# Kernel tuning notes

Hardware: AMD Instinct MI355X
Metric: run time of the kernel (lower is better)

Reference implementation:

```python
import jax, jax.numpy as jnp
import numpy as np

B, DIM, H, W = 4, 192, 256, 256
HEADS, DS = 6, 2
CPH = DIM // HEADS  # channels per head = 32
DN = ('NCHW', 'OIHW', 'NCHW')


def _conv(x, w, padding, groups=1):
    return jax.lax.conv_general_dilated(x, w, (1, 1), padding,
                                        dimension_numbers=DN,
                                        feature_group_count=groups)


def setup_inputs() -> dict:
    key = jax.random.key(0)
    ks = jax.random.split(key, 5)
    x = jax.random.normal(ks[0], (B, DIM, H, W), dtype=jnp.float32)
    temperature = jnp.ones((HEADS, 1, 1), dtype=jnp.float32)
    qkv_w = jax.random.normal(ks[1], (3 * DIM, DIM, 1, 1), dtype=jnp.float32) * 0.02
    dw_w = jax.random.normal(ks[2], (3 * DIM, 1, 3, 3), dtype=jnp.float32) * 0.02
    proj_w = jax.random.normal(ks[3], (DIM, DIM, 1, 1), dtype=jnp.float32) * 0.02
    a = jnp.full((1,), 0.2, dtype=jnp.float32)
    return {"x": x, "temperature": temperature, "qkv_w": qkv_w, "dw_w": dw_w,
            "proj_w": proj_w, "a1": a, "a2": a, "a3": a, "a4": a}


def _masked_softmax(attn, kk):
    # top-k mask per row (exact torch.topk + scatter_ semantics)
    _, idx = jax.lax.top_k(attn, kk)                      # [b,h,C,kk]
    mask = jax.nn.one_hot(idx, attn.shape[-1], dtype=jnp.bool_).any(axis=-2)
    return jax.nn.softmax(jnp.where(mask, attn, -jnp.inf), axis=-1)


def reference(x, temperature, qkv_w, dw_w, proj_w, a1, a2, a3, a4):
    b, c, h, w = x.shape
    h2, w2 = h // DS, w // DS
    # 1x1 qkv conv at full res, then exact adaptive (regular) max pool by DS
    qkv = _conv(x, qkv_w, 'VALID')                        # [b, 3*dim, h, w]
    qkv = jax.lax.reduce_window(qkv, -jnp.inf, jax.lax.max,
                                (1, 1, DS, DS), (1, 1, DS, DS), 'VALID')
    # depthwise 3x3
    qkv = _conv(qkv, dw_w, 'SAME', groups=3 * DIM)        # [b, 3*dim, h2, w2]
    q, k, v = jnp.split(qkv, 3, axis=1)
    n = h2 * w2
    q = q.reshape(b, HEADS, CPH, n)
    k = k.reshape(b, HEADS, CPH, n)
    v = v.reshape(b, HEADS, CPH, n)
    # F.normalize along last dim (eps clamp 1e-12)
    q = q / jnp.maximum(jnp.linalg.norm(q, axis=-1, keepdims=True), 1e-12)
    k = k / jnp.maximum(jnp.linalg.norm(k, axis=-1, keepdims=True), 1e-12)
    attn = jnp.einsum('bhcn,bhdn->bhcd', q, k) * temperature[None]  # [b,h,C,C]
    Cc = attn.shape[-1]
    att1 = _masked_softmax(attn, Cc // 2)
    att2 = _masked_softmax(attn, Cc * 2 // 3)
    att3 = _masked_softmax(attn, Cc * 3 // 4)
    att4 = _masked_softmax(attn, Cc * 4 // 5)
    def apply(a):
        return jnp.einsum('bhcd,bhdn->bhcn', a, v)
    out = apply(att1) * a1 + apply(att2) * a2 + apply(att3) * a3 + apply(att4) * a4
    out = out.reshape(b, DIM, h2, w2)
    out = jax.nn.gelu(out, approximate=False)
    # nearest upsample by integer factor DS
    out = jnp.repeat(jnp.repeat(out, DS, axis=2), DS, axis=3)
    out = _conv(out, proj_w, 'VALID')
    return out
```

## Files before the change

### kernel.cpp

```cpp
#include <hip/hip_runtime.h>
#include <hip/hip_bf16.h>
#include <math.h>

typedef __attribute__((ext_vector_type(8))) short bf16x8;
typedef __attribute__((ext_vector_type(4))) float f32x4;
typedef __attribute__((ext_vector_type(4))) unsigned int u32x4;

#define NP 16384
#define HWFULL 65536

__device__ __forceinline__ unsigned short f2bf(float f){
    union { float f; unsigned int u; } v; v.f = f;
    unsigned int u = v.u;
    u += 0x7fffu + ((u >> 16) & 1u);
    return (unsigned short)(u >> 16);
}
__device__ __forceinline__ float bf2f(unsigned short h){
    union { unsigned int u; float f; } v; v.u = ((unsigned int)h) << 16;
    return v.f;
}
__device__ __forceinline__ unsigned int pk2(float a, float b){
    unsigned int r;
    asm("v_cvt_pk_bf16_f32 %0, %1, %2" : "=v"(r) : "v"(a), "v"(b));
    return r;
}

__global__ void k_convert(const float* __restrict__ s, unsigned short* __restrict__ d, int n){
    int i = blockIdx.x * 256 + threadIdx.x;
    if (i < n) d[i] = f2bf(s[i]);
}

__global__ __launch_bounds__(256, 2)
void k_qkvpool(const float* __restrict__ x, const unsigned short* __restrict__ Wbf,
               unsigned short* __restrict__ qkvp){
    __shared__ unsigned short Bl[128*200];
    __shared__ unsigned short Ep[192*36];
    int tid = threadIdx.x;
    int lane = tid & 63, wv = tid >> 6;
    int n16 = lane & 15, quad = lane >> 4;
    int bx = blockIdx.x;
    int y2 = bx >> 2, x2blk = bx & 3;
    int b = blockIdx.y;

    #pragma unroll 6
    for (int j=0;j<12;j++){
        int idx = tid + j*256;
        int g = idx >> 7, w = idx & 127;
        int y = y2*2 + (w >> 6);
        int xc = x2blk*64 + (w & 63);
        const float* xp = x + (size_t)(b*192 + g*8) * HWFULL + y*256 + xc;
        float v0 = xp[0];
        float v1 = xp[(size_t)1*HWFULL];
        float v2 = xp[(size_t)2*HWFULL];
        float v3 = xp[(size_t)3*HWFULL];
        float v4 = xp[(size_t)4*HWFULL];
        float v5 = xp[(size_t)5*HWFULL];
        float v6 = xp[(size_t)6*HWFULL];
        float v7 = xp[(size_t)7*HWFULL];
        u32x4 pk;
        pk.x = pk2(v0,v1); pk.y = pk2(v2,v3); pk.z = pk2(v4,v5); pk.w = pk2(v6,v7);
        *(u32x4*)&Bl[w*200 + g*8] = pk;
    }
    bf16x8 afc[3], afn[3];
    #pragma unroll
    for (int j=0;j<3;j++)
        afc[j] = *(const bf16x8*)(Wbf + (size_t)(((wv*3+j)*16 + n16)*192 + quad*8));
    __syncthreads();

    for (int ocblk=0; ocblk<3; ocblk++){
        f32x4 acc[3][8];
        #pragma unroll
        for (int j=0;j<3;j++)
          #pragma unroll
          for (int s=0;s<8;s++)
            acc[j][s] = (f32x4){0.f,0.f,0.f,0.f};

        #pragma unroll 1
        for (int it=0; it<6; it++){
            int nocb = (it==5) ? ocblk+1 : ocblk;
            int nit  = (it==5) ? 0 : it+1;
            if (nocb < 3){
                #pragma unroll
                for (int j=0;j<3;j++)
                    afn[j] = *(const bf16x8*)(Wbf +
                        (size_t)((nocb*192 + (wv*3+j)*16 + n16)*192 + nit*32 + quad*8));
            }
            int bko = it*32 + quad*8;
            bf16x8 bfr[8];
            #pragma unroll
            for (int s=0;s<8;s++) bfr[s] = *(const bf16x8*)&Bl[(s*16 + n16)*200 + bko];
            #pragma unroll
            for (int j=0;j<3;j++)
              #pragma unroll
              for (int s=0;s<8;s++)
                acc[j][s] = __builtin_amdgcn_mfma_f32_16x16x32_bf16(afc[j], bfr[s], acc[j][s], 0,0,0);
            #pragma unroll
            for (int j=0;j<3;j++) afc[j] = afn[j];
        }
        __syncthreads();
        #pragma unroll
        for (int j=0;j<3;j++){
            int ocr = (wv*3+j)*16 + quad*4;
            #pragma unroll
            for (int sp=0;sp<4;sp++){
                #pragma unroll
                for (int r=0;r<4;r++){
                    float v = fmaxf(acc[j][sp][r], acc[j][sp+4][r]);
                    float o = __shfl_xor(v, 1, 64);
                    v = fmaxf(v, o);
                    if ((n16 & 1) == 0)
                        Ep[(ocr + r)*36 + sp*8 + (n16 >> 1)] = f2bf(v);
                }
            }
        }
        __syncthreads();
        size_t rowbase = (size_t)(b*576 + ocblk*192)*NP + y2*128 + x2blk*32;
        #pragma unroll
        for (int it2=0; it2<6; it2++){
            int c = tid + it2*256;
            int row = c >> 3, seg = c & 7;
            uint2 vv = *(const uint2*)&Ep[row*36 + seg*4];
            *(uint2*)(qkvp + rowbase + (size_t)row*NP + seg*4) = vv;
        }
    }
}

__global__ void k_dwconv(const unsigned short* __restrict__ qkvp, const float* __restrict__ dww,
                         unsigned short* __restrict__ dwoutB, float* __restrict__ sumsq){
    __shared__ float sl[18*132];
    int tid = threadIdx.x;
    int y0 = blockIdx.x * 16;
    int ch = blockIdx.y;
    int b  = blockIdx.z;
    const unsigned short* in = qkvp + (size_t)(b*576 + ch) * NP;
    int l = tid & 63, wr = tid >> 6;
    #pragma unroll
    for (int j=0;j<5;j++){
        int row = wr + j*4;
        if (row < 18){
            int gy = y0 - 1 + row;
            float2 v = make_float2(0.f, 0.f);
            if (gy >= 0 && gy < 128){
                unsigned int u = *(const unsigned int*)&in[gy*128 + l*2];
                v.x = bf2f((unsigned short)(u & 0xffffu));
                v.y = bf2f((unsigned short)(u >> 16));
            }
            *(float2*)&sl[row*132 + 2 + l*2] = v;
        }
    }
    if (tid < 18) sl[tid*132 + 1] = 0.f;
    else if (tid < 36) sl[(tid-18)*132 + 130] = 0.f;
    float w0 = dww[ch*9+0], w1 = dww[ch*9+1], w2 = dww[ch*9+2];
    float w3 = dww[ch*9+3], w4 = dww[ch*9+4], w5 = dww[ch*9+5];
    float w6 = dww[ch*9+6], w7 = dww[ch*9+7], w8 = dww[ch*9+8];
    __syncthreads();
    unsigned short* outp = dwoutB + (size_t)(b*576 + ch) * NP;
    int col = tid & 127, half = tid >> 7;
    float ssq = 0.f;
    int base = (half*8)*132 + col + 1;
    float r0a=sl[base],     r0b=sl[base+1],   r0c=sl[base+2];
    float r1a=sl[base+132], r1b=sl[base+133], r1c=sl[base+134];
    #pragma unroll
    for (int i=0;i<8;i++){
        const float* r2 = &sl[base + (i+2)*132];
        float r2a=r2[0], r2b=r2[1], r2c=r2[2];
        float a = r0a*w0 + r0b*w1 + r0c*w2
                + r1a*w3 + r1b*w4 + r1c*w5
                + r2a*w6 + r2b*w7 + r2c*w8;
        outp[(y0 + half*8 + i)*128 + col] = f2bf(a);
        ssq += a*a;
        r0a=r1a; r0b=r1b; r0c=r1c;
        r1a=r2a; r1b=r2b; r1c=r2c;
    }
    if (ch < 384){
        #pragma unroll
        for (int off=32; off>0; off>>=1) ssq += __shfl_down(ssq, off, 64);
        if ((tid & 63) == 0) atomicAdd(&sumsq[b*384 + ch], ssq);
    }
}

__global__ __launch_bounds__(256) void k_attnraw(const unsigned short* __restrict__ dwoutB,
                                                 float* __restrict__ attn){
    __shared__ float red[4][32][33];
    int tid = threadIdx.x;
    int lane = tid & 63, wv = tid >> 6;
    int n16 = lane & 15, quad = lane >> 4;
    int h = blockIdx.y, b = blockIdx.z;
    int n0 = blockIdx.x * 512 + wv * 128;
    const unsigned short* qb = dwoutB + (size_t)(b*576 + h*32)*NP;
    const unsigned short* kb = dwoutB + (size_t)(b*576 + 192 + h*32)*NP;

    f32x4 acc[2][2];
    #pragma unroll
    for (int i=0;i<2;i++)
      #pragma unroll
      for (int j=0;j<2;j++) acc[i][j] = (f32x4){0.f,0.f,0.f,0.f};

    #pragma unroll
    for (int ks=0; ks<4; ks++){
        int n = n0 + ks*32 + quad*8;
        bf16x8 aq0 = *(const bf16x8*)(qb + (size_t)(n16)*NP + n);
        bf16x8 aq1 = *(const bf16x8*)(qb + (size_t)(16 + n16)*NP + n);
        bf16x8 bk0 = *(const bf16x8*)(kb + (size_t)(n16)*NP + n);
        bf16x8 bk1 = *(const bf16x8*)(kb + (size_t)(16 + n16)*NP + n);
        acc[0][0] = __builtin_amdgcn_mfma_f32_16x16x32_bf16(aq0, bk0, acc[0][0], 0,0,0);
        acc[0][1] = __builtin_amdgcn_mfma_f32_16x16x32_bf16(aq0, bk1, acc[0][1], 0,0,0);
        acc[1][0] = __builtin_amdgcn_mfma_f32_16x16x32_bf16(aq1, bk0, acc[1][0], 0,0,0);
        acc[1][1] = __builtin_amdgcn_mfma_f32_16x16x32_bf16(aq1, bk1, acc[1][1], 0,0,0);
    }
    #pragma unroll
    for (int cc=0; cc<2; cc++)
      #pragma unroll
      for (int dd=0; dd<2; dd++)
        #pragma unroll
        for (int r=0; r<4; r++)
          red[wv][cc*16 + quad*4 + r][dd*16 + n16] = acc[cc][dd][r];
    __syncthreads();
    float* ap = attn + (size_t)(b*6+h)*1024;
    #pragma unroll
    for (int j=0;j<4;j++){
        int o = tid + j*256;
        int c = o >> 5, d = o & 31;
        float v = red[0][c][d] + red[1][c][d] + red[2][c][d] + red[3][c][d];
        atomicAdd(ap + o, v);
    }
}

__global__ void k_mask_softmax(const float* __restrict__ attn, const float* __restrict__ sumsq,
                               const float* __restrict__ temp,
                               const float* __restrict__ A1, const float* __restrict__ A2,
                               const float* __restrict__ A3, const float* __restrict__ A4,
                               float* __restrict__ comb){
    __shared__ float Am[32][33];
    __shared__ float qn[32], kn[32];
    int t = threadIdx.x;
    int bh = blockIdx.x;
    int b = bh / 6, h = bh % 6;
    if (t < 32) qn[t] = fmaxf(sqrtf(sumsq[b*384 + h*32 + t]), 1e-12f);
    else if (t >= 64 && t < 96) kn[t-64] = fmaxf(sqrtf(sumsq[b*384 + 192 + h*32 + (t-64)]), 1e-12f);
    __syncthreads();
    int c = t >> 5, d = t & 31;
    float tv = temp[h];
    float am = attn[(size_t)bh*1024 + t] * tv / (qn[c]*kn[d]);
    Am[c][d] = am;
    float m = am;
    #pragma unroll
    for (int off=16; off>0; off>>=1) m = fmaxf(m, __shfl_down(m, off, 32));
    m = __shfl(m, 0, 32);
    float e = expf(am - m);
    __syncthreads();
    int rk = 0;
    #pragma unroll 8
    for (int dd=0; dd<32; dd++){
        float av = Am[c][dd];
        rk += (av > am) || (av == am && dd < d);
    }
    float e0 = rk < 16 ? e : 0.f;
    float e1 = rk < 21 ? e : 0.f;
    float e2 = rk < 24 ? e : 0.f;
    float e3 = rk < 25 ? e : 0.f;
    #pragma unroll
    for (int off=16; off>0; off>>=1){
        e0 += __shfl_down(e0, off, 32);
        e1 += __shfl_down(e1, off, 32);
        e2 += __shfl_down(e2, off, 32);
        e3 += __shfl_down(e3, off, 32);
    }
    float d0 = __shfl(e0, 0, 32), d1 = __shfl(e1, 0, 32);
    float d2 = __shfl(e2, 0, 32), d3 = __shfl(e3, 0, 32);
    float s = (rk<16 ? A1[0]/d0 : 0.f) + (rk<21 ? A2[0]/d1 : 0.f)
            + (rk<24 ? A3[0]/d2 : 0.f) + (rk<25 ? A4[0]/d3 : 0.f);
    comb[(size_t)bh*1024 + t] = e * s;
}

__global__ void k_applyv(const unsigned short* __restrict__ dwoutB, const float* __restrict__ comb,
                         unsigned short* __restrict__ gT){
    __shared__ float cm[3072];
    int tid = threadIdx.x;
    int b = blockIdx.y;
    int hz = blockIdx.z * 3;
    int n = blockIdx.x*256 + tid;
    #pragma unroll
    for (int j=0;j<12;j++) cm[tid + j*256] = comb[b*6144 + hz*1024 + tid + j*256];
    __syncthreads();
    const unsigned short* vb = dwoutB + (size_t)(b*576 + 384 + hz*32)*NP + n;
    unsigned short* gp = gT + (size_t)(b*NP + n)*192 + hz*32;
    #pragma unroll 1
    for (int h=0;h<3;h++){
        float v[32];
        #pragma unroll
        for (int d=0;d<32;d++) v[d] = bf2f(vb[(size_t)(h*32+d)*NP]);
        const float* chp = &cm[h*1024];
        #pragma unroll 1
        for (int cg=0;cg<4;cg++){
            float s[8];
            #pragma unroll
            for (int i=0;i<8;i++){
                const float* crow = chp + (cg*8+i)*32;
                float acc = 0.f;
                #pragma unroll
                for (int d=0;d<32;d++) acc += crow[d]*v[d];
                s[i] = 0.5f*acc*(1.f + erff(acc*0.70710678118654752f));
            }
            u32x4 pk;
            pk.x = pk2(s[0],s[1]); pk.y = pk2(s[2],s[3]);
            pk.z = pk2(s[4],s[5]); pk.w = pk2(s[6],s[7]);
            *(u32x4*)(gp + h*32 + cg*8) = pk;
        }
    }
}

__global__ __launch_bounds__(256, 2)
void k_proj(const unsigned short* __restrict__ gT, const unsigned short* __restrict__ Pbf,
            float* __restrict__ out){
    __shared__ unsigned short Bl[128*200];
    int tid = threadIdx.x;
    int lane = tid & 63, wv = tid >> 6;
    int n16 = lane & 15, quad = lane >> 4;
    int y2 = blockIdx.x, b = blockIdx.y;

    #pragma unroll 6
    for (int j=0;j<12;j++){
        int idx = tid + j*256;
        int r = idx / 24, g = idx - r*24;
        *(u32x4*)&Bl[r*200 + g*8] =
            *(const u32x4*)(gT + ((size_t)(b*NP + y2*128 + r)*192 + g*8));
    }
    bf16x8 afc[3], afn[3];
    #pragma unroll
    for (int j=0;j<3;j++)
        afc[j] = *(const bf16x8*)(Pbf + (size_t)(((wv*3+j)*16 + n16)*192 + quad*8));
    __syncthreads();

    f32x4 acc[3][8];
    #pragma unroll
    for (int j=0;j<3;j++)
      #pragma unroll
      for (int s=0;s<8;s++)
        acc[j][s] = (f32x4){0.f,0.f,0.f,0.f};

    #pragma unroll 1
    for (int it=0; it<6; it++){
        if (it < 5){
            #pragma unroll
            for (int j=0;j<3;j++)
                afn[j] = *(const bf16x8*)(Pbf +
                    (size_t)(((wv*3+j)*16 + n16)*192 + (it+1)*32 + quad*8));
        }
        int bko = it*32 + quad*8;
        bf16x8 bfr[8];
        #pragma unroll
        for (int s=0;s<8;s++) bfr[s] = *(const bf16x8*)&Bl[(s*16 + n16)*200 + bko];
        #pragma unroll
        for (int j=0;j<3;j++)
          #pragma unroll
          for (int s=0;s<8;s++)
            acc[j][s] = __builtin_amdgcn_mfma_f32_16x16x32_bf16(afc[j], bfr[s], acc[j][s], 0,0,0);
        #pragma unroll
        for (int j=0;j<3;j++) afc[j] = afn[j];
    }

    #pragma unroll
    for (int j=0;j<3;j++){
        int oc = (wv*3+j)*16 + quad*4;
        #pragma unroll
        for (int sp=0;sp<8;sp++){
            int x2 = sp*16 + n16;
            #pragma unroll
            for (int r=0;r<4;r++){
                float v = acc[j][sp][r];
                size_t o = ((size_t)(b*192 + oc + r)*256 + 2*y2)*256 + 2*x2;
                float2 val = make_float2(v, v);
                *(float2*)(out + o) = val;
                *(float2*)(out + o + 256) = val;
            }
        }
    }
}

extern "C" void kernel_launch(void* const* d_in, const int* in_sizes, int n_in,
                              void* d_out, int out_size, void* d_ws, size_t ws_size,
                              hipStream_t stream){
    const float* x     = (const float*)d_in[0];
    const float* temp  = (const float*)d_in[1];
    const float* qkvw  = (const float*)d_in[2];
    const float* dww   = (const float*)d_in[3];
    const float* projw = (const float*)d_in[4];
    const float* A1    = (const float*)d_in[5];
    const float* A2    = (const float*)d_in[6];
    const float* A3    = (const float*)d_in[7];
    const float* A4    = (const float*)d_in[8];
    float* out = (float*)d_out;
    char* ws = (char*)d_ws;

    unsigned short* dwoutB = (unsigned short*)ws;
    unsigned short* qkvp   = (unsigned short*)(ws + 75497472ull);
    unsigned short* gT     = (unsigned short*)(ws + 75497472ull);
    unsigned short* Wbf    = (unsigned short*)(ws + 150994944ull);
    unsigned short* Pbf    = (unsigned short*)(ws + 151216128ull);
    float*          attn   = (float*)(ws + 151289856ull);
    float*          comb   = (float*)(ws + 151388160ull);
    float*          sumsq  = (float*)(ws + 151486464ull);

    hipMemsetAsync(attn, 0, 98304, stream);
    hipMemsetAsync(sumsq, 0, 6144, stream);
    k_convert<<<dim3((110592+255)/256), dim3(256), 0, stream>>>(qkvw, Wbf, 110592);
    k_convert<<<dim3((36864+255)/256), dim3(256), 0, stream>>>(projw, Pbf, 36864);
    k_qkvpool<<<dim3(512,4), dim3(256), 0, stream>>>(x, Wbf, qkvp);
    k_dwconv<<<dim3(8,576,4), dim3(256), 0, stream>>>(qkvp, dww, dwoutB, sumsq);
    k_attnraw<<<dim3(32,6,4), dim3(256), 0, stream>>>(dwoutB, attn);
    k_mask_softmax<<<dim3(24), dim3(1024), 0, stream>>>(attn, sumsq, temp, A1, A2, A3, A4, comb);
    k_applyv<<<dim3(64,4,2), dim3(256), 0, stream>>>(dwoutB, comb, gT);
    k_proj<<<dim3(128,4), dim3(256), 0, stream>>>(gT, Pbf, out);
}
```

Measured before the change: 564.0 us.

## Fuse attention-apply-V with projection GEMM and merge weight conversion kernels

Merges the attention-times-V plus GELU kernel into the projection kernel. Each block computes its 128-pixel tile of GELU outputs directly into shared memory, so the bf16 gT intermediate is no longer written to and re-read from global memory. The two weight-conversion launches are also combined into one. The cost is that the fused kernel now holds a 24KB comb table in shared memory and runs fewer blocks (512) for the apply-V part, which may lower parallelism for that phase.

```diff
diff --git a/kernel.cpp b/kernel.cpp
--- a/kernel.cpp
+++ b/kernel.cpp
@@ -25,9 +25,11 @@
     return r;
 }
 
-__global__ void k_convert(const float* __restrict__ s, unsigned short* __restrict__ d, int n){
+__global__ void k_convert2(const float* __restrict__ qw, const float* __restrict__ pw,
+                           unsigned short* __restrict__ Wbf, unsigned short* __restrict__ Pbf){
     int i = blockIdx.x * 256 + threadIdx.x;
-    if (i < n) d[i] = f2bf(s[i]);
+    if (i < 110592) Wbf[i] = f2bf(qw[i]);
+    else if (i < 110592 + 36864) Pbf[i - 110592] = f2bf(pw[i - 110592]);
 }
 
 __global__ __launch_bounds__(256, 2)
@@ -273,26 +275,28 @@
     comb[(size_t)bh*1024 + t] = e * s;
 }
 
-__global__ void k_applyv(const unsigned short* __restrict__ dwoutB, const float* __restrict__ comb,
-                         unsigned short* __restrict__ gT){
-    __shared__ float cm[3072];
+__global__ __launch_bounds__(256, 2)
+void k_avproj(const unsigned short* __restrict__ dwoutB, const float* __restrict__ comb,
+              const unsigned short* __restrict__ Pbf, float* __restrict__ out){
+    __shared__ unsigned short Bl[128*200];
+    __shared__ float cm[6144];
     int tid = threadIdx.x;
-    int b = blockIdx.y;
-    int hz = blockIdx.z * 3;
-    int n = blockIdx.x*256 + tid;
-    #pragma unroll
-    for (int j=0;j<12;j++) cm[tid + j*256] = comb[b*6144 + hz*1024 + tid + j*256];
-    __syncthreads();
-    const unsigned short* vb = dwoutB + (size_t)(b*576 + 384 + hz*32)*NP + n;
-    unsigned short* gp = gT + (size_t)(b*NP + n)*192 + hz*32;
+    int y2 = blockIdx.x, b = blockIdx.y;
+
+    #pragma unroll
+    for (int j=0;j<24;j++) cm[tid + j*256] = comb[b*6144 + tid + j*256];
+
+    int n_loc = tid & 127, half = tid >> 7;
+    const unsigned short* vb = dwoutB + (size_t)(b*576 + 384 + half*96)*NP + y2*128 + n_loc;
+    __syncthreads();
     #pragma unroll 1
-    for (int h=0;h<3;h++){
+    for (int hh=0; hh<3; hh++){
         float v[32];
         #pragma unroll
-        for (int d=0;d<32;d++) v[d] = bf2f(vb[(size_t)(h*32+d)*NP]);
-        const float* chp = &cm[h*1024];
+        for (int d=0; d<32; d++) v[d] = bf2f(vb[(size_t)(hh*32+d)*NP]);
+        const float* chp = &cm[(half*3+hh)*1024];
         #pragma unroll 1
-        for (int cg=0;cg<4;cg++){
+        for (int cg=0; cg<4; cg++){
             float s[8];
             #pragma unroll
             for (int i=0;i<8;i++){
@@ -305,27 +309,12 @@
             u32x4 pk;
             pk.x = pk2(s[0],s[1]); pk.y = pk2(s[2],s[3]);
             pk.z = pk2(s[4],s[5]); pk.w = pk2(s[6],s[7]);
-            *(u32x4*)(gp + h*32 + cg*8) = pk;
-        }
-    }
-}
-
-__global__ __launch_bounds__(256, 2)
-void k_proj(const unsigned short* __restrict__ gT, const unsigned short* __restrict__ Pbf,
-            float* __restrict__ out){
-    __shared__ unsigned short Bl[128*200];
-    int tid = threadIdx.x;
+            *(u32x4*)&Bl[n_loc*200 + half*96 + hh*32 + cg*8] = pk;
+        }
+    }
+
     int lane = tid & 63, wv = tid >> 6;
     int n16 = lane & 15, quad = lane >> 4;
-    int y2 = blockIdx.x, b = blockIdx.y;
-
-    #pragma unroll 6
-    for (int j=0;j<12;j++){
-        int idx = tid + j*256;
-        int r = idx / 24, g = idx - r*24;
-        *(u32x4*)&Bl[r*200 + g*8] =
-            *(const u32x4*)(gT + ((size_t)(b*NP + y2*128 + r)*192 + g*8));
-    }
     bf16x8 afc[3], afn[3];
     #pragma unroll
     for (int j=0;j<3;j++)
@@ -395,7 +384,6 @@
 
     unsigned short* dwoutB = (unsigned short*)ws;
     unsigned short* qkvp   = (unsigned short*)(ws + 75497472ull);
-    unsigned short* gT     = (unsigned short*)(ws + 75497472ull);
     unsigned short* Wbf    = (unsigned short*)(ws + 150994944ull);
     unsigned short* Pbf    = (unsigned short*)(ws + 151216128ull);
     float*          attn   = (float*)(ws + 151289856ull);
@@ -404,12 +392,10 @@
 
     hipMemsetAsync(attn, 0, 98304, stream);
     hipMemsetAsync(sumsq, 0, 6144, stream);
-    k_convert<<<dim3((110592+255)/256), dim3(256), 0, stream>>>(qkvw, Wbf, 110592);
-    k_convert<<<dim3((36864+255)/256), dim3(256), 0, stream>>>(projw, Pbf, 36864);
+    k_convert2<<<dim3((147456+255)/256), dim3(256), 0, stream>>>(qkvw, projw, Wbf, Pbf);
     k_qkvpool<<<dim3(512,4), dim3(256), 0, stream>>>(x, Wbf, qkvp);
     k_dwconv<<<dim3(8,576,4), dim3(256), 0, stream>>>(qkvp, dww, dwoutB, sumsq);
     k_attnraw<<<dim3(32,6,4), dim3(256), 0, stream>>>(dwoutB, attn);
     k_mask_softmax<<<dim3(24), dim3(1024), 0, stream>>>(attn, sumsq, temp, A1, A2, A3, A4, comb);
-    k_applyv<<<dim3(64,4,2), dim3(256), 0, stream>>>(dwoutB, comb, gT);
-    k_proj<<<dim3(128,4), dim3(256), 0, stream>>>(gT, Pbf, out);
-}
+    k_avproj<<<dim3(128,4), dim3(256), 0, stream>>>(dwoutB, comb, Pbf, out);
+}
```

New measurement: 546.4 us. 1.03x faster.
